# Kernel optimization log

Hardware: AMD Instinct MI355X
Metric: run time of the kernel (lower is better)

## Reference

```python
import jax, jax.numpy as jnp
import numpy as np

# Module constants (from init_kwargs): 2D domain, m=[1024,1024], omega=[0,1,0,1]
PAD = 2
M0, M1 = 1024, 1024
OMEGA_LO = np.array([0.0, 0.0], dtype=np.float32)   # omega[0::2]
H = np.array([1.0 / 1024.0, 1.0 / 1024.0], dtype=np.float32)  # (omega_hi-omega_lo)/m
N_POINTS = 2097152


def _b0(j, xi):
    # Cubic B-spline basis pieces, exactly as SplineInter.b0
    if j == 1:
        return (2 + xi) * (2 + xi) * (2 + xi)
    elif j == 2:
        return -(3 * xi + 6) * (xi * xi) + 4
    elif j == 3:
        return (3 * xi - 6) * (xi * xi) + 4
    elif j == 4:
        return (2 - xi) * (2 - xi) * (2 - xi)


def _basis(t):
    # t: [N] fractional part; returns [N,4] weights for offsets j=-1,0,1,2
    # matches b0(3 - j, t - j)
    return jnp.stack([_b0(3 - j, t - j) for j in range(-1, 3)], axis=-1)


def setup_inputs() -> dict:
    key = jax.random.key(0)
    k1, k2 = jax.random.split(key)
    # query points in physical domain [0,1)^2 -> normalized coords in [-0.5, 1023.5)
    x = jax.random.uniform(k1, (N_POINTS, 2), dtype=jnp.float32)
    # padded spline coefficient grid: (M0+2*PAD, M1+2*PAD)
    coeffs = 0.1 * jax.random.normal(k2, (M0 + 2 * PAD, M1 + 2 * PAD), dtype=jnp.float32)
    return {"x": x, "coeffs": coeffs}


def reference(x, coeffs):
    x = x.reshape(-1, 2)
    # normalize to grid coords
    xn = (x - jnp.asarray(OMEGA_LO)) / jnp.asarray(H) - 0.5  # [N,2]
    m = jnp.array([M0, M1], dtype=xn.dtype)
    valid = jnp.all((xn > -2) & (xn < m), axis=1)            # [N]
    P = jnp.floor(xn).astype(jnp.int32)                      # [N,2]
    t = xn - P                                               # fractional part [N,2]

    i1 = M1 + 2 * PAD  # row stride of padded coeff grid
    p = i1 * (PAD + P[:, 0]) + (PAD + P[:, 1])               # [N] base flat index

    w0 = _basis(t[:, 0])  # [N,4]
    w1 = _basis(t[:, 1])  # [N,4]

    js = jnp.arange(-1, 3, dtype=jnp.int32)
    idx = p[:, None, None] + js[:, None] * i1 + js[None, :]  # [N,4,4]
    cflat = coeffs.reshape(-1)
    safe_idx = jnp.clip(idx, 0, cflat.shape[0] - 1)
    vals = cflat[safe_idx]                                   # [N,4,4] gathered stencil

    out = jnp.einsum('nij,ni,nj->n', vals, w0, w1)
    out = jnp.where(valid, out, 0.0)
    return out[:, None]  # [N,1]
```

## Files before the change

### kernel.cpp

```cpp
#include <hip/hip_runtime.h>


#define I1 1028
#define TOTAL (1028 * 1028)

typedef float f4u __attribute__((ext_vector_type(4), aligned(4)));

__device__ __forceinline__ void basis4(float t, float w[4]) {
    float a = 1.0f - t;
    w[0] = a * a * a;
    w[1] = (3.0f * t - 6.0f) * (t * t) + 4.0f;
    float xi = t - 1.0f;
    w[2] = -(3.0f * xi + 6.0f) * (xi * xi) + 4.0f;
    w[3] = t * t * t;
}

__global__ __launch_bounds__(256) void spline_1pt_kernel(
    const float* __restrict__ x,
    const float* __restrict__ coeffs,
    float* __restrict__ out,
    int n)
{
    int i = blockIdx.x * blockDim.x + threadIdx.x;
    if (i >= n) return;

    float2 xy = reinterpret_cast<const float2*>(x)[i];

    float xn0 = xy.x * 1024.0f - 0.5f;
    float xn1 = xy.y * 1024.0f - 0.5f;

    bool valid = (xn0 > -2.0f) && (xn0 < 1024.0f) &&
                 (xn1 > -2.0f) && (xn1 < 1024.0f);

    float P0f = floorf(xn0);
    float P1f = floorf(xn1);
    int P0 = (int)P0f;
    int P1 = (int)P1f;
    float t0 = xn0 - P0f;
    float t1 = xn1 - P1f;

    int base = I1 * (2 + P0) + (2 + P1);
    int r0 = P0 + 1;
    int c0 = P1 + 1;
    bool interior = (r0 >= 0) && (r0 <= 1024) && (c0 >= 0) && (c0 <= 1024);

    float acc;
    if (interior) {
        const float* rowp = coeffs + base - I1 - 1;
        f4u v0 = *reinterpret_cast<const f4u*>(rowp);
        f4u v1 = *reinterpret_cast<const f4u*>(rowp + I1);
        f4u v2 = *reinterpret_cast<const f4u*>(rowp + 2 * I1);
        f4u v3 = *reinterpret_cast<const f4u*>(rowp + 3 * I1);

        float w0[4], w1[4];
        basis4(t0, w0);
        basis4(t1, w1);

        float s0 = fmaf(v0.x, w1[0], fmaf(v0.y, w1[1],
                   fmaf(v0.z, w1[2], v0.w * w1[3])));
        float s1 = fmaf(v1.x, w1[0], fmaf(v1.y, w1[1],
                   fmaf(v1.z, w1[2], v1.w * w1[3])));
        float s2 = fmaf(v2.x, w1[0], fmaf(v2.y, w1[1],
                   fmaf(v2.z, w1[2], v2.w * w1[3])));
        float s3 = fmaf(v3.x, w1[0], fmaf(v3.y, w1[1],
                   fmaf(v3.z, w1[2], v3.w * w1[3])));

        acc = fmaf(s0, w0[0], fmaf(s1, w0[1], fmaf(s2, w0[2], s3 * w0[3])));
    } else {
        float w0[4], w1[4];
        basis4(t0, w0);
        basis4(t1, w1);
        acc = 0.0f;
#pragma unroll
        for (int j = 0; j < 4; ++j) {
            int r = base + (j - 1) * I1 - 1;
            float s = 0.0f;
#pragma unroll
            for (int k = 0; k < 4; ++k) {
                int idx = r + k;
                idx = min(max(idx, 0), TOTAL - 1);
                s = fmaf(coeffs[idx], w1[k], s);
            }
            acc = fmaf(s, w0[j], acc);
        }
    }

    out[i] = valid ? acc : 0.0f;
}

extern "C" void kernel_launch(void* const* d_in, const int* in_sizes, int n_in,
                              void* d_out, int out_size, void* d_ws, size_t ws_size,
                              hipStream_t stream) {
    const float* x = (const float*)d_in[0];
    const float* coeffs = (const float*)d_in[1];
    float* out = (float*)d_out;

    int n = in_sizes[0] / 2;

    int block = 256;
    int grid = (n + block - 1) / block;
    spline_1pt_kernel<<<grid, block, 0, stream>>>(x, coeffs, out, n);
}
```

Measured before the change: 110.8 us.

## Pre-pack 4x4 coefficient stencils as fp16 tiles for single-line gathers

Adds a pack kernel that rebuilds the padded coefficient grid into per-position 4x4 stencils stored as fp16, 32 bytes each. The eval kernel can then fetch each point's whole stencil with two 16-byte loads from one contiguous block instead of four unaligned row loads. This is meant to cut scattered cache-line traffic per random query point. In exchange it adds a pack pass over a roughly 34 MB workspace buffer every call, and it lowers coefficient precision to fp16, which may exceed tolerance.

```diff
diff --git a/kernel.cpp b/kernel.cpp
--- a/kernel.cpp
+++ b/kernel.cpp
@@ -1,8 +1,13 @@
 #include <hip/hip_runtime.h>
+#include <hip/hip_fp16.h>
 
 
 #define I1 1028
 #define TOTAL (1028 * 1028)
+#define NG 257
+#define LPC (NG * NG)
+#define NPACK (4 * LPC)
+#define NTILES (16 * LPC)
 
 typedef float f4u __attribute__((ext_vector_type(4), aligned(4)));
 
@@ -15,17 +20,157 @@
     w[3] = t * t * t;
 }
 
+__device__ __forceinline__ float2 h2f(unsigned int u) {
+    __half2 h = *reinterpret_cast<__half2*>(&u);
+    return __half22float2(h);
+}
+
+
+__global__ __launch_bounds__(256) void pack_h16_kernel(
+    const float* __restrict__ coeffs, uint4* __restrict__ Q)
+{
+    int t = blockIdx.x * blockDim.x + threadIdx.x;
+    if (t >= NPACK) return;
+    int p   = t / LPC;
+    int rem = t - p * LPC;
+    int i   = rem / NG;
+    int j   = rem - i * NG;
+    int rb  = 4 * i + p;
+    int cb  = 4 * j;
+
+    const float* R[4];
+#pragma unroll
+    for (int r = 0; r < 4; ++r)
+        R[r] = coeffs + min(rb + r, 1027) * I1;
+
+    float c[4][8];
+    if (cb + 7 <= 1027) {
+#pragma unroll
+        for (int r = 0; r < 4; ++r) {
+            f4u a = *reinterpret_cast<const f4u*>(R[r] + cb);
+            f4u b = *reinterpret_cast<const f4u*>(R[r] + cb + 4);
+            c[r][0] = a.x; c[r][1] = a.y; c[r][2] = a.z; c[r][3] = a.w;
+            c[r][4] = b.x; c[r][5] = b.y; c[r][6] = b.z; c[r][7] = b.w;
+        }
+    } else {
+#pragma unroll
+        for (int r = 0; r < 4; ++r)
+#pragma unroll
+            for (int k = 0; k < 8; ++k)
+                c[r][k] = R[r][min(cb + k, 1027)];
+    }
+
+    unsigned short h[8][4];
+#pragma unroll
+    for (int k = 0; k < 8; ++k)
+#pragma unroll
+        for (int r = 0; r < 4; ++r)
+            h[k][r] = __half_as_ushort(__float2half(c[r][k]));
+
+#pragma unroll
+    for (int q = 0; q < 4; ++q) {
+        int line = (p * 4 + q) * LPC + i * NG + j;
+        uint4 lo, hi;
+        lo.x = (unsigned)h[q + 0][0] | ((unsigned)h[q + 0][1] << 16);
+        lo.y = (unsigned)h[q + 0][2] | ((unsigned)h[q + 0][3] << 16);
+        lo.z = (unsigned)h[q + 1][0] | ((unsigned)h[q + 1][1] << 16);
+        lo.w = (unsigned)h[q + 1][2] | ((unsigned)h[q + 1][3] << 16);
+        hi.x = (unsigned)h[q + 2][0] | ((unsigned)h[q + 2][1] << 16);
+        hi.y = (unsigned)h[q + 2][2] | ((unsigned)h[q + 2][3] << 16);
+        hi.z = (unsigned)h[q + 3][0] | ((unsigned)h[q + 3][1] << 16);
+        hi.w = (unsigned)h[q + 3][2] | ((unsigned)h[q + 3][3] << 16);
+        Q[2 * line]     = lo;
+        Q[2 * line + 1] = hi;
+    }
+}
+
+
+__global__ __launch_bounds__(256) void eval_h16_kernel(
+    const float* __restrict__ x,
+    const float* __restrict__ coeffs,
+    const uint4* __restrict__ Q,
+    float* __restrict__ out, int n)
+{
+    int i = blockIdx.x * blockDim.x + threadIdx.x;
+    if (i >= n) return;
+
+    float2 xy = reinterpret_cast<const float2*>(x)[i];
+    float xn0 = xy.x * 1024.0f - 0.5f;
+    float xn1 = xy.y * 1024.0f - 0.5f;
+
+    bool valid = (xn0 > -2.0f) && (xn0 < 1024.0f) &&
+                 (xn1 > -2.0f) && (xn1 < 1024.0f);
+
+    float P0f = floorf(xn0);
+    float P1f = floorf(xn1);
+    int P0 = (int)P0f;
+    int P1 = (int)P1f;
+    float t0 = xn0 - P0f;
+    float t1 = xn1 - P1f;
+
+    int r0 = P0 + 1;
+    int c0 = P1 + 1;
+    bool interior = (r0 >= 0) && (r0 <= 1024) && (c0 >= 0) && (c0 <= 1024);
+
+    float acc;
+    if (interior) {
+        int line = ((r0 & 3) * 4 + (c0 & 3)) * LPC + (r0 >> 2) * NG + (c0 >> 2);
+        uint4 lo = Q[2 * line];
+        uint4 hi = Q[2 * line + 1];
+
+        float w0[4], w1[4];
+        basis4(t0, w0);
+        basis4(t1, w1);
+
+        float2 a, b;
+        a = h2f(lo.x); b = h2f(lo.y);
+        float cs0 = fmaf(a.x, w0[0], fmaf(a.y, w0[1],
+                    fmaf(b.x, w0[2], b.y * w0[3])));
+        a = h2f(lo.z); b = h2f(lo.w);
+        float cs1 = fmaf(a.x, w0[0], fmaf(a.y, w0[1],
+                    fmaf(b.x, w0[2], b.y * w0[3])));
+        a = h2f(hi.x); b = h2f(hi.y);
+        float cs2 = fmaf(a.x, w0[0], fmaf(a.y, w0[1],
+                    fmaf(b.x, w0[2], b.y * w0[3])));
+        a = h2f(hi.z); b = h2f(hi.w);
+        float cs3 = fmaf(a.x, w0[0], fmaf(a.y, w0[1],
+                    fmaf(b.x, w0[2], b.y * w0[3])));
+
+        acc = fmaf(cs0, w1[0], fmaf(cs1, w1[1],
+              fmaf(cs2, w1[2], cs3 * w1[3])));
+    } else {
+        float w0[4], w1[4];
+        basis4(t0, w0);
+        basis4(t1, w1);
+        int base = I1 * (2 + P0) + (2 + P1);
+        acc = 0.0f;
+#pragma unroll
+        for (int j = 0; j < 4; ++j) {
+            int r = base + (j - 1) * I1 - 1;
+            float s = 0.0f;
+#pragma unroll
+            for (int k = 0; k < 4; ++k) {
+                int idx = r + k;
+                idx = min(max(idx, 0), TOTAL - 1);
+                s = fmaf(coeffs[idx], w1[k], s);
+            }
+            acc = fmaf(s, w0[j], acc);
+        }
+    }
+
+    out[i] = valid ? acc : 0.0f;
+}
+
+
 __global__ __launch_bounds__(256) void spline_1pt_kernel(
     const float* __restrict__ x,
     const float* __restrict__ coeffs,
-    float* __restrict__ out,
-    int n)
+    float* __restrict__ out, int n)
 {
     int i = blockIdx.x * blockDim.x + threadIdx.x;
     if (i >= n) return;
 
     float2 xy = reinterpret_cast<const float2*>(x)[i];
-
     float xn0 = xy.x * 1024.0f - 0.5f;
     float xn1 = xy.y * 1024.0f - 0.5f;
 
@@ -56,14 +201,10 @@
         basis4(t0, w0);
         basis4(t1, w1);
 
-        float s0 = fmaf(v0.x, w1[0], fmaf(v0.y, w1[1],
-                   fmaf(v0.z, w1[2], v0.w * w1[3])));
-        float s1 = fmaf(v1.x, w1[0], fmaf(v1.y, w1[1],
-                   fmaf(v1.z, w1[2], v1.w * w1[3])));
-        float s2 = fmaf(v2.x, w1[0], fmaf(v2.y, w1[1],
-                   fmaf(v2.z, w1[2], v2.w * w1[3])));
-        float s3 = fmaf(v3.x, w1[0], fmaf(v3.y, w1[1],
-                   fmaf(v3.z, w1[2], v3.w * w1[3])));
+        float s0 = fmaf(v0.x, w1[0], fmaf(v0.y, w1[1], fmaf(v0.z, w1[2], v0.w * w1[3])));
+        float s1 = fmaf(v1.x, w1[0], fmaf(v1.y, w1[1], fmaf(v1.z, w1[2], v1.w * w1[3])));
+        float s2 = fmaf(v2.x, w1[0], fmaf(v2.y, w1[1], fmaf(v2.z, w1[2], v2.w * w1[3])));
+        float s3 = fmaf(v3.x, w1[0], fmaf(v3.y, w1[1], fmaf(v3.z, w1[2], v3.w * w1[3])));
 
         acc = fmaf(s0, w0[0], fmaf(s1, w0[1], fmaf(s2, w0[2], s3 * w0[3])));
     } else {
@@ -88,6 +229,7 @@
     out[i] = valid ? acc : 0.0f;
 }
 
+
 extern "C" void kernel_launch(void* const* d_in, const int* in_sizes, int n_in,
                               void* d_out, int out_size, void* d_ws, size_t ws_size,
                               hipStream_t stream) {
@@ -97,7 +239,19 @@
 
     int n = in_sizes[0] / 2;
 
-    int block = 256;
-    int grid = (n + block - 1) / block;
-    spline_1pt_kernel<<<grid, block, 0, stream>>>(x, coeffs, out, n);
-}
+    size_t need = (size_t)NTILES * 32;
+
+    if (ws_size >= need) {
+        uint4* Q = (uint4*)d_ws;
+
+        int gpack = (NPACK + 255) / 256;
+        pack_h16_kernel<<<gpack, 256, 0, stream>>>(coeffs, Q);
+
+        int geval = (n + 255) / 256;
+        eval_h16_kernel<<<geval, 256, 0, stream>>>(x, coeffs, Q, out, n);
+    } else {
+        int block = 256;
+        int grid = (n + block - 1) / block;
+        spline_1pt_kernel<<<grid, block, 0, stream>>>(x, coeffs, out, n);
+    }
+}
```

Result: no change. 109.8 us (-0.9%).

## Repack coefficients into fp16 row-quads for fewer gather loads

Applied to the files above, without the earlier changes.

Adds a pre-pass that converts the coefficient grid to fp16 and interleaves groups of four rows per column into 8-byte elements. The eval kernel then covers the 4x4 stencil with two 16-byte loads from each of two quad-rows, using shifted row weights, in place of four unaligned row loads. It also uses nontemporal loads and stores for the streaming input and output. This trades an extra pack kernel each call and fp16 precision loss on the coefficients for less gather traffic and fewer memory transactions.

```diff
diff --git a/kernel.cpp b/kernel.cpp
--- a/kernel.cpp
+++ b/kernel.cpp
@@ -1,10 +1,15 @@
 #include <hip/hip_runtime.h>
+#include <hip/hip_fp16.h>
 
 
 #define I1 1028
 #define TOTAL (1028 * 1028)
+#define NQ 258
+#define QELEMS (NQ * I1)
 
 typedef float f4u __attribute__((ext_vector_type(4), aligned(4)));
+typedef float f2v __attribute__((ext_vector_type(2)));
+typedef unsigned int u4a8 __attribute__((ext_vector_type(4), aligned(8)));
 
 __device__ __forceinline__ void basis4(float t, float w[4]) {
     float a = 1.0f - t;
@@ -15,17 +20,146 @@
     w[3] = t * t * t;
 }
 
+__device__ __forceinline__ float2 h2f(unsigned int u) {
+    __half2 h = *reinterpret_cast<__half2*>(&u);
+    return __half22float2(h);
+}
+
+__device__ __forceinline__ void shifted_w8(const float w0[4], int s, float W[8]) {
+#pragma unroll
+    for (int t = 0; t < 8; ++t) {
+        float v = 0.0f;
+        if (t - 0 >= 0 && t - 0 < 4) v = (s == 0) ? w0[t - 0] : v;
+        if (t - 1 >= 0 && t - 1 < 4) v = (s == 1) ? w0[t - 1] : v;
+        if (t - 2 >= 0 && t - 2 < 4) v = (s == 2) ? w0[t - 2] : v;
+        if (t - 3 >= 0 && t - 3 < 4) v = (s == 3) ? w0[t - 3] : v;
+        W[t] = v;
+    }
+}
+
+__device__ __forceinline__ float col8(unsigned a01, unsigned a23,
+                                      unsigned b01, unsigned b23,
+                                      const float W[8]) {
+    float2 p0 = h2f(a01);
+    float2 p1 = h2f(a23);
+    float2 p2 = h2f(b01);
+    float2 p3 = h2f(b23);
+    return fmaf(p0.x, W[0], fmaf(p0.y, W[1],
+           fmaf(p1.x, W[2], fmaf(p1.y, W[3],
+           fmaf(p2.x, W[4], fmaf(p2.y, W[5],
+           fmaf(p3.x, W[6], p3.y * W[7])))))));
+}
+
+
+__global__ __launch_bounds__(256) void pack_f16q_kernel(
+    const float* __restrict__ coeffs, uint2* __restrict__ QH)
+{
+    int t = blockIdx.x * blockDim.x + threadIdx.x;
+    if (t >= QELEMS) return;
+    int qi = t / I1;
+    int c  = t - qi * I1;
+    int rb = 4 * qi;
+    float v0 = coeffs[min(rb + 0, 1027) * I1 + c];
+    float v1 = coeffs[min(rb + 1, 1027) * I1 + c];
+    float v2 = coeffs[min(rb + 2, 1027) * I1 + c];
+    float v3 = coeffs[min(rb + 3, 1027) * I1 + c];
+    unsigned h0 = __half_as_ushort(__float2half(v0));
+    unsigned h1 = __half_as_ushort(__float2half(v1));
+    unsigned h2 = __half_as_ushort(__float2half(v2));
+    unsigned h3 = __half_as_ushort(__float2half(v3));
+    uint2 e;
+    e.x = h0 | (h1 << 16);
+    e.y = h2 | (h3 << 16);
+    QH[t] = e;
+}
+
+
+__global__ __launch_bounds__(256) void eval_f16q_kernel(
+    const float* __restrict__ x,
+    const float* __restrict__ coeffs,
+    const ushort* __restrict__ QH,
+    float* __restrict__ out, int n)
+{
+    int i = blockIdx.x * blockDim.x + threadIdx.x;
+    if (i >= n) return;
+
+    f2v xy = __builtin_nontemporal_load(reinterpret_cast<const f2v*>(x) + i);
+
+    float xn0 = xy.x * 1024.0f - 0.5f;
+    float xn1 = xy.y * 1024.0f - 0.5f;
+
+    bool valid = (xn0 > -2.0f) && (xn0 < 1024.0f) &&
+                 (xn1 > -2.0f) && (xn1 < 1024.0f);
+
+    float P0f = floorf(xn0);
+    float P1f = floorf(xn1);
+    int P0 = (int)P0f;
+    int P1 = (int)P1f;
+    float t0 = xn0 - P0f;
+    float t1 = xn1 - P1f;
+
+    int r0 = P0 + 1;
+    int c0 = P1 + 1;
+    bool interior = (r0 >= 0) && (r0 <= 1024) && (c0 >= 0) && (c0 <= 1024);
+
+    float acc;
+    if (interior) {
+        int s  = r0 & 3;
+        int qi = r0 >> 2;
+        const ushort* pA = QH + (size_t)(qi * I1 + c0) * 4;
+        const ushort* pB = pA + (size_t)I1 * 4;
+        u4a8 A0 = *reinterpret_cast<const u4a8*>(pA);
+        u4a8 A1 = *reinterpret_cast<const u4a8*>(pA + 8);
+        u4a8 B0 = *reinterpret_cast<const u4a8*>(pB);
+        u4a8 B1 = *reinterpret_cast<const u4a8*>(pB + 8);
+
+        float w0[4], w1[4];
+        basis4(t0, w0);
+        basis4(t1, w1);
+        float W[8];
+        shifted_w8(w0, s, W);
+
+        float cs0 = col8(A0.x, A0.y, B0.x, B0.y, W);
+        float cs1 = col8(A0.z, A0.w, B0.z, B0.w, W);
+        float cs2 = col8(A1.x, A1.y, B1.x, B1.y, W);
+        float cs3 = col8(A1.z, A1.w, B1.z, B1.w, W);
+
+        acc = fmaf(cs0, w1[0], fmaf(cs1, w1[1],
+              fmaf(cs2, w1[2], cs3 * w1[3])));
+    } else {
+        float w0[4], w1[4];
+        basis4(t0, w0);
+        basis4(t1, w1);
+        int base = I1 * (2 + P0) + (2 + P1);
+        acc = 0.0f;
+#pragma unroll
+        for (int j = 0; j < 4; ++j) {
+            int r = base + (j - 1) * I1 - 1;
+            float sum = 0.0f;
+#pragma unroll
+            for (int k = 0; k < 4; ++k) {
+                int idx = r + k;
+                idx = min(max(idx, 0), TOTAL - 1);
+                sum = fmaf(coeffs[idx], w1[k], sum);
+            }
+            acc = fmaf(sum, w0[j], acc);
+        }
+    }
+
+    float result = valid ? acc : 0.0f;
+    __builtin_nontemporal_store(result, &out[i]);
+}
+
+
 __global__ __launch_bounds__(256) void spline_1pt_kernel(
     const float* __restrict__ x,
     const float* __restrict__ coeffs,
-    float* __restrict__ out,
-    int n)
+    float* __restrict__ out, int n)
 {
     int i = blockIdx.x * blockDim.x + threadIdx.x;
     if (i >= n) return;
 
     float2 xy = reinterpret_cast<const float2*>(x)[i];
-
     float xn0 = xy.x * 1024.0f - 0.5f;
     float xn1 = xy.y * 1024.0f - 0.5f;
 
@@ -56,14 +190,10 @@
         basis4(t0, w0);
         basis4(t1, w1);
 
-        float s0 = fmaf(v0.x, w1[0], fmaf(v0.y, w1[1],
-                   fmaf(v0.z, w1[2], v0.w * w1[3])));
-        float s1 = fmaf(v1.x, w1[0], fmaf(v1.y, w1[1],
-                   fmaf(v1.z, w1[2], v1.w * w1[3])));
-        float s2 = fmaf(v2.x, w1[0], fmaf(v2.y, w1[1],
-                   fmaf(v2.z, w1[2], v2.w * w1[3])));
-        float s3 = fmaf(v3.x, w1[0], fmaf(v3.y, w1[1],
-                   fmaf(v3.z, w1[2], v3.w * w1[3])));
+        float s0 = fmaf(v0.x, w1[0], fmaf(v0.y, w1[1], fmaf(v0.z, w1[2], v0.w * w1[3])));
+        float s1 = fmaf(v1.x, w1[0], fmaf(v1.y, w1[1], fmaf(v1.z, w1[2], v1.w * w1[3])));
+        float s2 = fmaf(v2.x, w1[0], fmaf(v2.y, w1[1], fmaf(v2.z, w1[2], v2.w * w1[3])));
+        float s3 = fmaf(v3.x, w1[0], fmaf(v3.y, w1[1], fmaf(v3.z, w1[2], v3.w * w1[3])));
 
         acc = fmaf(s0, w0[0], fmaf(s1, w0[1], fmaf(s2, w0[2], s3 * w0[3])));
     } else {
@@ -88,6 +218,7 @@
     out[i] = valid ? acc : 0.0f;
 }
 
+
 extern "C" void kernel_launch(void* const* d_in, const int* in_sizes, int n_in,
                               void* d_out, int out_size, void* d_ws, size_t ws_size,
                               hipStream_t stream) {
@@ -97,7 +228,20 @@
 
     int n = in_sizes[0] / 2;
 
-    int block = 256;
-    int grid = (n + block - 1) / block;
-    spline_1pt_kernel<<<grid, block, 0, stream>>>(x, coeffs, out, n);
-}
+    size_t need = (size_t)QELEMS * 8;
+
+    if (ws_size >= need) {
+        uint2* QH = (uint2*)d_ws;
+
+        int gpack = (QELEMS + 255) / 256;
+        pack_f16q_kernel<<<gpack, 256, 0, stream>>>(coeffs, QH);
+
+        int geval = (n + 255) / 256;
+        eval_f16q_kernel<<<geval, 256, 0, stream>>>(
+            x, coeffs, (const ushort*)QH, out, n);
+    } else {
+        int block = 256;
+        int grid = (n + block - 1) / block;
+        spline_1pt_kernel<<<grid, block, 0, stream>>>(x, coeffs, out, n);
+    }
+}
```

Result: faster. 92.16 us (median of 2 runs) (-16.8%).
